# Optimization experiments

Measured on AMD Instinct MI355X. Metric: run time of the kernel, lower is better.

Reference implementation:

```python
import jax, jax.numpy as jnp
import numpy as np

ALPHA = 0.2            # LeakyReLU negative slope
NEG_BIG = -9e15        # mask fill value from the original code


def setup_inputs() -> dict:
    key = jax.random.key(0)
    k1, k2, k3, k4 = jax.random.split(key, 4)
    N, F_in, F_out = 8192, 512, 256
    x = jax.random.normal(k1, (N, F_in), dtype=jnp.float32)
    support = jax.random.randint(k2, (N, N), 0, 2, dtype=jnp.int32)  # dense 0/1 adjacency
    W = jax.random.normal(k3, (F_in, F_out), dtype=jnp.float32) * (1.0 / np.sqrt(F_in))
    a = jax.random.normal(k4, (2 * F_out, 1), dtype=jnp.float32) * 0.05
    return {"x": x, "support": support, "W": W, "a": a}


def _attention_logits(h, a):
    # Faithful reproduction of the ORIGINAL (buggy) torch layout:
    #   a_input = cat([h.repeat(1,N).view(N*N,-1), h.repeat(N,1)], dim=0).view(N, N, 2F)
    # Working out the flat-index arithmetic (N even):
    #   for i <  N/2: a_input[i,j] = concat(h[q], h[q]),  q = 2*i + (j >= N/2)
    #   for i >= N/2: a_input[i,j] = concat(h[(2j) % N], h[(2j+1) % N])   (independent of i)
    # so e_raw[i,j] = a_input[i,j] @ a decomposes via s = h@a1, t = h@a2.
    N, F = h.shape
    a1 = a[:F, 0]
    a2 = a[F:, 0]
    s = h @ a1                     # (N,)
    t = h @ a2                     # (N,)
    u = s + t
    half = N // 2
    j = jnp.arange(N)
    i_top = jnp.arange(half)
    q = 2 * i_top[:, None] + (j[None, :] >= half).astype(jnp.int32)  # (half, N)
    top = u[q]                                                       # rows i < N/2
    bot = s[(2 * j) % N] + t[(2 * j + 1) % N]                        # (N,) same for all i >= N/2
    e_raw = jnp.concatenate([top, jnp.broadcast_to(bot, (N - half, N))], axis=0)
    return jnp.where(e_raw > 0, e_raw, ALPHA * e_raw)  # LeakyReLU


def reference(x, support, W, a):
    h = x @ W                                  # (N, F_out)
    e = _attention_logits(h, a)                # (N, N)
    scores = jnp.where(support > 0, e, jnp.float32(NEG_BIG))
    attn = jax.nn.softmax(scores, axis=1)      # dropout p=0.0 -> identity
    h_out = attn @ h                           # (N, F_out)
    return jax.nn.elu(h_out)                   # concat=True
```

## Files before the change

kernel.cpp:

```cpp
#include <hip/hip_runtime.h>


typedef short bf16x8 __attribute__((ext_vector_type(8)));
typedef float f32x4 __attribute__((ext_vector_type(4)));

static __device__ __forceinline__ unsigned short f2bf(float f) {
    unsigned int u = __builtin_bit_cast(unsigned int, f);
    unsigned int r = (u + 0x7FFFu + ((u >> 16) & 1u)) >> 16;
    return (unsigned short)r;
}
static __device__ __forceinline__ float bf2f(unsigned short s) {
    unsigned int u = ((unsigned int)s) << 16;
    return __builtin_bit_cast(float, u);
}

__global__ __launch_bounds__(256) void k_cvt_x(const float* __restrict__ x,
                                               unsigned short* __restrict__ xb) {
    int i = (blockIdx.x * 256 + threadIdx.x) * 4;
    float4 v = *(const float4*)(x + i);
    ushort4 o = make_ushort4(f2bf(v.x), f2bf(v.y), f2bf(v.z), f2bf(v.w));
    *(ushort4*)(xb + i) = o;
}

__global__ __launch_bounds__(256) void k_cvt_w(const float* __restrict__ W,
                                               unsigned short* __restrict__ Wbt) {
    int idx = blockIdx.x * 256 + threadIdx.x;
    int n = idx >> 9, k = idx & 511;
    Wbt[idx] = f2bf(W[k * 256 + n]);
}

__global__ __launch_bounds__(256) void k_gemm_h(const unsigned short* __restrict__ xb,
                                                const unsigned short* __restrict__ Wbt,
                                                unsigned short* __restrict__ h,
                                                unsigned short* __restrict__ B1t) {
    __shared__ unsigned short Asm[128][72];
    __shared__ unsigned short Bsm[64][72];
    int tid = threadIdx.x;
    int wv = tid >> 6, ln = tid & 63;
    int m0 = blockIdx.x * 128, n0 = blockIdx.y * 64;

    f32x4 acc[2][4];
#pragma unroll
    for (int i = 0; i < 2; i++)
#pragma unroll
        for (int j = 0; j < 4; j++) acc[i][j] = (f32x4)0.0f;

    for (int k0 = 0; k0 < 512; k0 += 64) {
        {
            int r = tid >> 1, c = (tid & 1) * 32;
            const unsigned short* src = xb + (m0 + r) * 512 + k0 + c;
            *(bf16x8*)&Asm[r][c]      = *(const bf16x8*)(src);
            *(bf16x8*)&Asm[r][c + 8]  = *(const bf16x8*)(src + 8);
            *(bf16x8*)&Asm[r][c + 16] = *(const bf16x8*)(src + 16);
            *(bf16x8*)&Asm[r][c + 24] = *(const bf16x8*)(src + 24);
        }
        {
            int r = tid >> 2, c = (tid & 3) * 16;
            const unsigned short* src = Wbt + (n0 + r) * 512 + k0 + c;
            *(bf16x8*)&Bsm[r][c]     = *(const bf16x8*)(src);
            *(bf16x8*)&Bsm[r][c + 8] = *(const bf16x8*)(src + 8);
        }
        __syncthreads();
        int lr = ln & 15, lk = (ln >> 4) * 8;
#pragma unroll
        for (int ks = 0; ks < 2; ks++) {
            int kk = ks * 32 + lk;
            bf16x8 a0 = *(const bf16x8*)&Asm[wv * 32 + lr][kk];
            bf16x8 a1 = *(const bf16x8*)&Asm[wv * 32 + 16 + lr][kk];
#pragma unroll
            for (int nt = 0; nt < 4; nt++) {
                bf16x8 b = *(const bf16x8*)&Bsm[nt * 16 + lr][kk];
                acc[0][nt] = __builtin_amdgcn_mfma_f32_16x16x32_bf16(a0, b, acc[0][nt], 0, 0, 0);
                acc[1][nt] = __builtin_amdgcn_mfma_f32_16x16x32_bf16(a1, b, acc[1][nt], 0, 0, 0);
            }
        }
        __syncthreads();
    }
    int lr = ln & 15, lrow = (ln >> 4) * 4;
#pragma unroll
    for (int mt = 0; mt < 2; mt++) {
#pragma unroll
        for (int nt = 0; nt < 4; nt++) {
            int mg = m0 + wv * 32 + mt * 16 + lrow;
            int ng = n0 + nt * 16 + lr;
            ushort4 tb = make_ushort4(f2bf(acc[mt][nt][0]), f2bf(acc[mt][nt][1]),
                                      f2bf(acc[mt][nt][2]), f2bf(acc[mt][nt][3]));
            h[(mg + 0) * 256 + ng] = tb.x;
            h[(mg + 1) * 256 + ng] = tb.y;
            h[(mg + 2) * 256 + ng] = tb.z;
            h[(mg + 3) * 256 + ng] = tb.w;
            *(ushort4*)&B1t[ng * 8192 + mg] = tb;
        }
    }
}

__global__ __launch_bounds__(256) void k_st(const unsigned short* __restrict__ h,
                                            const float* __restrict__ a,
                                            float* __restrict__ s, float* __restrict__ t) {
    int wv = threadIdx.x >> 6, ln = threadIdx.x & 63;
    int j = blockIdx.x * 4 + wv;
    ushort4 hv = *(const ushort4*)(h + j * 256 + ln * 4);
    float4 a1 = *(const float4*)(a + ln * 4);
    float4 a2 = *(const float4*)(a + 256 + ln * 4);
    float s_ = bf2f(hv.x) * a1.x + bf2f(hv.y) * a1.y + bf2f(hv.z) * a1.z + bf2f(hv.w) * a1.w;
    float t_ = bf2f(hv.x) * a2.x + bf2f(hv.y) * a2.y + bf2f(hv.z) * a2.z + bf2f(hv.w) * a2.w;
#pragma unroll
    for (int off = 32; off; off >>= 1) {
        s_ += __shfl_down(s_, off);
        t_ += __shfl_down(t_, off);
    }
    if (ln == 0) { s[j] = s_; t[j] = t_; }
}

__global__ __launch_bounds__(256) void k_weights(const float* __restrict__ s,
                                                 const float* __restrict__ t,
                                                 float* __restrict__ wb,
                                                 float* __restrict__ eL,
                                                 float* __restrict__ eR,
                                                 unsigned short* __restrict__ B1t) {
    int j = blockIdx.x * 256 + threadIdx.x;
    float eb = s[(2 * j) & 8191] + t[(2 * j + 1) & 8191];
    eb = eb > 0.0f ? eb : 0.2f * eb;
    wb[j] = expf(eb);
    if (j < 4096) {
        float cL = s[2 * j] + t[2 * j];
        cL = cL > 0.0f ? cL : 0.2f * cL;
        float cR = s[2 * j + 1] + t[2 * j + 1];
        cR = cR > 0.0f ? cR : 0.2f * cR;
        eL[j] = expf(cL);
        eR[j] = expf(cR);
    }
    B1t[256 * 8192 + j] = 0x3F80;
#pragma unroll
    for (int f = 257; f < 272; f++) B1t[f * 8192 + j] = 0;
}

__global__ __launch_bounds__(256) void k_b2(const unsigned short* __restrict__ B1t,
                                            const float* __restrict__ wb,
                                            unsigned short* __restrict__ B2t) {
    int j = blockIdx.x * 256 + threadIdx.x;
    int f = blockIdx.y;
    B2t[f * 8192 + j] = f2bf(wb[j] * bf2f(B1t[f * 8192 + j]));
}

static __device__ __forceinline__ bf16x8 cvt01(int4 a, int4 b) {
    bf16x8 r;
    r[0] = a.x ? (short)0x3F80 : (short)0; r[1] = a.y ? (short)0x3F80 : (short)0;
    r[2] = a.z ? (short)0x3F80 : (short)0; r[3] = a.w ? (short)0x3F80 : (short)0;
    r[4] = b.x ? (short)0x3F80 : (short)0; r[5] = b.y ? (short)0x3F80 : (short)0;
    r[6] = b.z ? (short)0x3F80 : (short)0; r[7] = b.w ? (short)0x3F80 : (short)0;
    return r;
}

template <int NF>
static __device__ __forceinline__ void mg_body(unsigned short* __restrict__ As,
                                               const int* __restrict__ asrc,
                                               int arow, int acx,
                                               const unsigned short* __restrict__ bp,
                                               float* __restrict__ op, int ln) {
    f32x4 acc[2][NF];
#pragma unroll
    for (int i = 0; i < 2; i++)
#pragma unroll
        for (int j = 0; j < NF; j++) acc[i][j] = (f32x4)0.0f;

    {
        int4 a0 = *(const int4*)(asrc);
        int4 a1 = *(const int4*)(asrc + 4);
        *(bf16x8*)&As[arow * 72 + acx] = cvt01(a0, a1);
    }
    int r0 = (ln & 15), r1 = 16 + (ln & 15), lk = (ln >> 4) * 8;

#pragma unroll 1
    for (int it = 0; it < 32; ++it) {
        __syncthreads();
        int4 na0, na1;
        if (it < 31) {
            const int* a2 = asrc + (it + 1) * 64;
            na0 = *(const int4*)(a2);
            na1 = *(const int4*)(a2 + 4);
        }
        int base = (it & 1) * 32 * 72;
#pragma unroll
        for (int kh = 0; kh < 2; kh++) {
            bf16x8 af0 = *(const bf16x8*)&As[base + r0 * 72 + kh * 32 + lk];
            bf16x8 af1 = *(const bf16x8*)&As[base + r1 * 72 + kh * 32 + lk];
#pragma unroll
            for (int f = 0; f < NF; f++) {
                bf16x8 bv = *(const bf16x8*)(bp + (long)f * 131072 + it * 64 + kh * 32);
                acc[0][f] = __builtin_amdgcn_mfma_f32_16x16x32_bf16(af0, bv, acc[0][f], 0, 0, 0);
                acc[1][f] = __builtin_amdgcn_mfma_f32_16x16x32_bf16(af1, bv, acc[1][f], 0, 0, 0);
            }
        }
        if (it < 31) {
            int nb = ((it & 1) ^ 1) * 32 * 72;
            *(bf16x8*)&As[nb + arow * 72 + acx] = cvt01(na0, na1);
        }
    }
    int lr = ln & 15, lrow = (ln >> 4) * 4;
#pragma unroll
    for (int mf = 0; mf < 2; mf++)
#pragma unroll
        for (int f = 0; f < NF; f++)
#pragma unroll
            for (int r = 0; r < 4; r++)
                unsafeAtomicAdd(&op[(long)(mf * 16 + lrow + r) * 272 + f * 16 + lr],
                                acc[mf][f][r]);
}

__global__ __launch_bounds__(256, 4) void k_mgemm(const int* __restrict__ sup,
                                                  const unsigned short* __restrict__ B1t,
                                                  const unsigned short* __restrict__ B2t,
                                                  float* __restrict__ TL, float* __restrict__ TR,
                                                  float* __restrict__ TB0, float* __restrict__ TB1) {
    __shared__ unsigned short Asm[2 * 32 * 72];
    int tid = threadIdx.x;
    int wv = tid >> 6, ln = tid & 63;

    int bid = blockIdx.x + (blockIdx.y << 8);
    int xcd = bid & 7;
    int idx = bid >> 3;
    int q = xcd >> 1;
    int strip = (idx << 1) | (xcd & 1);

    bool topv = strip < 128;
    long m0 = (long)strip * 32;
    const unsigned short* Bt = topv ? B1t : B2t;
    float* out = topv ? ((q < 2) ? TL : TR) : ((q < 2) ? TB0 : TB1);
    long outr0 = topv ? m0 : m0 - 4096;
    long K0 = (long)q * 2048;
    int n0 = wv ? (4 * wv + 1) * 16 : 0;

    int arow = tid >> 3, acx = (tid & 7) * 8;
    const int* asrc = sup + (m0 + arow) * 8192 + K0 + acx;
    const unsigned short* bp = Bt + (long)(n0 + (ln & 15)) * 8192 + K0 + (ln >> 4) * 8;
    float* op = out + outr0 * 272 + n0;

    if (wv == 0) mg_body<5>(Asm, asrc, arow, acx, bp, op, ln);
    else         mg_body<4>(Asm, asrc, arow, acx, bp, op, ln);
}

__global__ __launch_bounds__(256) void k_out(const float* __restrict__ TL,
                                             const float* __restrict__ TR,
                                             const float* __restrict__ TB0,
                                             const float* __restrict__ TB1,
                                             const float* __restrict__ eL,
                                             const float* __restrict__ eR,
                                             float* __restrict__ outp) {
    int i = blockIdx.x, f = threadIdx.x;
    float num, den;
    if (i < 4096) {
        float el = eL[i], er = eR[i];
        den = el * TL[i * 272 + 256] + er * TR[i * 272 + 256];
        num = el * TL[i * 272 + f] + er * TR[i * 272 + f];
    } else {
        int ii = i - 4096;
        den = TB0[ii * 272 + 256] + TB1[ii * 272 + 256];
        num = TB0[ii * 272 + f] + TB1[ii * 272 + f];
    }
    float r = num / den;
    outp[i * 256 + f] = r > 0.0f ? r : expm1f(r);
}

extern "C" void kernel_launch(void* const* d_in, const int* in_sizes, int n_in,
                              void* d_out, int out_size, void* d_ws, size_t ws_size,
                              hipStream_t stream) {
    (void)in_sizes; (void)n_in; (void)out_size; (void)ws_size;
    const float* x = (const float*)d_in[0];
    const int* sup = (const int*)d_in[1];
    const float* W = (const float*)d_in[2];
    const float* a = (const float*)d_in[3];
    float* outp = (float*)d_out;

    char* ws = (char*)d_ws;
    size_t off = 0;
    auto alloc = [&](size_t bytes) -> void* {
        void* p = ws + off;
        off += (bytes + 255) & ~(size_t)255;
        return p;
    };
    unsigned short* xb  = (unsigned short*)alloc(8192 * 512 * 2);
    unsigned short* Wbt = (unsigned short*)alloc(256 * 512 * 2);
    unsigned short* h   = (unsigned short*)alloc(8192 * 256 * 2);
    unsigned short* B1t = (unsigned short*)alloc(272 * 8192 * 2);
    unsigned short* B2t = (unsigned short*)alloc(272 * 8192 * 2);
    float* s   = (float*)alloc(8192 * 4);
    float* t   = (float*)alloc(8192 * 4);
    float* wb  = (float*)alloc(8192 * 4);
    float* eL  = (float*)alloc(4096 * 4);
    float* eR  = (float*)alloc(4096 * 4);
    float* TL  = (float*)alloc(4096 * 272 * 4);
    float* TR  = (float*)alloc(4096 * 272 * 4);
    float* TB0 = (float*)alloc(4096 * 272 * 4);
    float* TB1 = (float*)alloc(4096 * 272 * 4);

    hipMemsetAsync(TL, 0, (size_t)4 * 4096 * 272 * 4, stream);

    k_cvt_x<<<4096, 256, 0, stream>>>(x, xb);
    k_cvt_w<<<512, 256, 0, stream>>>(W, Wbt);
    k_gemm_h<<<dim3(64, 4), 256, 0, stream>>>(xb, Wbt, h, B1t);
    k_st<<<2048, 256, 0, stream>>>(h, a, s, t);
    k_weights<<<32, 256, 0, stream>>>(s, t, wb, eL, eR, B1t);
    k_b2<<<dim3(32, 272), 256, 0, stream>>>(B1t, wb, B2t);
    k_mgemm<<<dim3(256, 4), 256, 0, stream>>>(sup, B1t, B2t, TL, TR, TB0, TB1);
    k_out<<<8192, 256, 0, stream>>>(TL, TR, TB0, TB1, eL, eR, outp);
}
```

Baseline: 212.0 us.

## Restructure mask GEMM: stage B via direct-to-LDS loads, split-K partials without atomics

The masked GEMM is restructured so each block handles a 64-row strip over a 1024-wide K slice. The B operand (272 columns) is staged in swizzled, double-buffered LDS using global_load_lds, and each wave converts its own adjacency fragment straight from registers. Atomic accumulation into four zero-initialized buffers is replaced by plain stores into 8 split-K partial buffers, which k_out then sums, so the memset goes away. The cost is a larger workspace and more reads in k_out, plus higher register pressure from 17 accumulators per wave.

```diff
diff --git a/kernel.cpp b/kernel.cpp
--- a/kernel.cpp
+++ b/kernel.cpp
@@ -12,6 +12,11 @@
 static __device__ __forceinline__ float bf2f(unsigned short s) {
     unsigned int u = ((unsigned int)s) << 16;
     return __builtin_bit_cast(float, u);
+}
+static __device__ __forceinline__ void glds16(const unsigned short* g, unsigned short* l) {
+    __builtin_amdgcn_global_load_lds(
+        (const __attribute__((address_space(1))) unsigned int*)(g),
+        (__attribute__((address_space(3))) unsigned int*)(l), 16, 0, 0);
 }
 
 __global__ __launch_bounds__(256) void k_cvt_x(const float* __restrict__ x,
@@ -152,114 +157,129 @@
     return r;
 }
 
-template <int NF>
-static __device__ __forceinline__ void mg_body(unsigned short* __restrict__ As,
-                                               const int* __restrict__ asrc,
-                                               int arow, int acx,
-                                               const unsigned short* __restrict__ bp,
-                                               float* __restrict__ op, int ln) {
-    f32x4 acc[2][NF];
-#pragma unroll
-    for (int i = 0; i < 2; i++)
-#pragma unroll
-        for (int j = 0; j < NF; j++) acc[i][j] = (f32x4)0.0f;
-
-    {
-        int4 a0 = *(const int4*)(asrc);
-        int4 a1 = *(const int4*)(asrc + 4);
-        *(bf16x8*)&As[arow * 72 + acx] = cvt01(a0, a1);
-    }
-    int r0 = (ln & 15), r1 = 16 + (ln & 15), lk = (ln >> 4) * 8;
-
-#pragma unroll 1
-    for (int it = 0; it < 32; ++it) {
-        __syncthreads();
-        int4 na0, na1;
-        if (it < 31) {
-            const int* a2 = asrc + (it + 1) * 64;
-            na0 = *(const int4*)(a2);
-            na1 = *(const int4*)(a2 + 4);
-        }
-        int base = (it & 1) * 32 * 72;
-#pragma unroll
-        for (int kh = 0; kh < 2; kh++) {
-            bf16x8 af0 = *(const bf16x8*)&As[base + r0 * 72 + kh * 32 + lk];
-            bf16x8 af1 = *(const bf16x8*)&As[base + r1 * 72 + kh * 32 + lk];
-#pragma unroll
-            for (int f = 0; f < NF; f++) {
-                bf16x8 bv = *(const bf16x8*)(bp + (long)f * 131072 + it * 64 + kh * 32);
-                acc[0][f] = __builtin_amdgcn_mfma_f32_16x16x32_bf16(af0, bv, acc[0][f], 0, 0, 0);
-                acc[1][f] = __builtin_amdgcn_mfma_f32_16x16x32_bf16(af1, bv, acc[1][f], 0, 0, 0);
-            }
-        }
-        if (it < 31) {
-            int nb = ((it & 1) ^ 1) * 32 * 72;
-            *(bf16x8*)&As[nb + arow * 72 + acx] = cvt01(na0, na1);
-        }
-    }
-    int lr = ln & 15, lrow = (ln >> 4) * 4;
-#pragma unroll
-    for (int mf = 0; mf < 2; mf++)
-#pragma unroll
-        for (int f = 0; f < NF; f++)
-#pragma unroll
-            for (int r = 0; r < 4; r++)
-                unsafeAtomicAdd(&op[(long)(mf * 16 + lrow + r) * 272 + f * 16 + lr],
-                                acc[mf][f][r]);
-}
-
 __global__ __launch_bounds__(256, 4) void k_mgemm(const int* __restrict__ sup,
                                                   const unsigned short* __restrict__ B1t,
                                                   const unsigned short* __restrict__ B2t,
-                                                  float* __restrict__ TL, float* __restrict__ TR,
-                                                  float* __restrict__ TB0, float* __restrict__ TB1) {
-    __shared__ unsigned short Asm[2 * 32 * 72];
-    int tid = threadIdx.x;
-    int wv = tid >> 6, ln = tid & 63;
-
-    int bid = blockIdx.x + (blockIdx.y << 8);
-    int xcd = bid & 7;
-    int idx = bid >> 3;
-    int q = xcd >> 1;
-    int strip = (idx << 1) | (xcd & 1);
-
-    bool topv = strip < 128;
-    long m0 = (long)strip * 32;
-    const unsigned short* Bt = topv ? B1t : B2t;
-    float* out = topv ? ((q < 2) ? TL : TR) : ((q < 2) ? TB0 : TB1);
-    long outr0 = topv ? m0 : m0 - 4096;
-    long K0 = (long)q * 2048;
-    int n0 = wv ? (4 * wv + 1) * 16 : 0;
-
-    int arow = tid >> 3, acx = (tid & 7) * 8;
-    const int* asrc = sup + (m0 + arow) * 8192 + K0 + acx;
-    const unsigned short* bp = Bt + (long)(n0 + (ln & 15)) * 8192 + K0 + (ln >> 4) * 8;
-    float* op = out + outr0 * 272 + n0;
-
-    if (wv == 0) mg_body<5>(Asm, asrc, arow, acx, bp, op, ln);
-    else         mg_body<4>(Asm, asrc, arow, acx, bp, op, ln);
-}
-
-__global__ __launch_bounds__(256) void k_out(const float* __restrict__ TL,
-                                             const float* __restrict__ TR,
-                                             const float* __restrict__ TB0,
-                                             const float* __restrict__ TB1,
+                                                  float* __restrict__ P) {
+    __shared__ unsigned short Bsm[2 * 8704];
+    int tid = threadIdx.x, wv = tid >> 6, ln = tid & 63;
+    int bid = blockIdx.x;
+    int q = bid & 7;
+    int strip = bid >> 3;
+    long K0 = (long)q * 1024;
+    long m0 = (long)strip * 64;
+    const unsigned short* Bt = (strip < 64) ? B1t : B2t;
+
+    const unsigned short* sp0; const unsigned short* sp1;
+    const unsigned short* sp2; const unsigned short* sp3;
+    const unsigned short* sp4;
+    int cb0, cb1, cb2, cb3, cb4;
+    {
+        int ch;
+#define SETUP_SP(I, SP, CB) \
+        ch = (I)*256 + wv*64 + ln; \
+        { int row = ch >> 2, c = ch & 3; \
+          CB = ((I)*256 + wv*64) * 8; \
+          SP = Bt + (long)row * 8192 + K0 + ((c ^ (row & 3)) << 3); }
+        SETUP_SP(0, sp0, cb0)
+        SETUP_SP(1, sp1, cb1)
+        SETUP_SP(2, sp2, cb2)
+        SETUP_SP(3, sp3, cb3)
+        ch = 1024 + ln;
+        { int row = ch >> 2, c = ch & 3;
+          cb4 = 1024 * 8;
+          sp4 = Bt + (long)row * 8192 + K0 + ((c ^ (row & 3)) << 3); }
+#undef SETUP_SP
+    }
+
+    const int* ap = sup + (m0 + wv * 16 + (ln & 15)) * 8192 + K0 + (ln >> 4) * 8;
+
+    f32x4 acc[17];
+#pragma unroll
+    for (int i = 0; i < 17; i++) acc[i] = (f32x4)0.0f;
+
+    {
+        unsigned short* dst = Bsm;
+        glds16(sp0, dst + cb0);
+        glds16(sp1, dst + cb1);
+        glds16(sp2, dst + cb2);
+        glds16(sp3, dst + cb3);
+        if (wv == 0) glds16(sp4, dst + cb4);
+    }
+    int4 c0 = *(const int4*)(ap);
+    int4 c1 = *(const int4*)(ap + 4);
+    int4 n0 = *(const int4*)(ap + 32);
+    int4 n1 = *(const int4*)(ap + 36);
+    int4 f0 = c0, f1 = c1;
+    asm volatile("s_waitcnt vmcnt(4)" ::: "memory");
+    __builtin_amdgcn_s_barrier();
+
+    int lr = ln & 15;
+    int swz16 = 16 * ((ln >> 4) ^ (ln & 3));
+
+#pragma unroll 1
+    for (int it = 0; it < 32; ++it) {
+        int buf = it & 1;
+        if (it < 31) {
+            unsigned short* dst = Bsm + (buf ^ 1) * 8704;
+            glds16(sp0 + (it + 1) * 32, dst + cb0);
+            glds16(sp1 + (it + 1) * 32, dst + cb1);
+            glds16(sp2 + (it + 1) * 32, dst + cb2);
+            glds16(sp3 + (it + 1) * 32, dst + cb3);
+            if (wv == 0) glds16(sp4 + (it + 1) * 32, dst + cb4);
+        }
+        if (it < 30) {
+            f0 = *(const int4*)(ap + (it + 2) * 32);
+            f1 = *(const int4*)(ap + (it + 2) * 32 + 4);
+        }
+        bf16x8 av = cvt01(c0, c1);
+        const char* base = (const char*)Bsm + buf * 17408 + 64 * lr + swz16;
+#pragma unroll
+        for (int f = 0; f < 17; f++) {
+            bf16x8 bv = *(const bf16x8*)(base + f * 1024);
+            acc[f] = __builtin_amdgcn_mfma_f32_16x16x32_bf16(av, bv, acc[f], 0, 0, 0);
+        }
+        c0 = n0; c1 = n1; n0 = f0; n1 = f1;
+        if (it < 31) {
+            if (it < 30) asm volatile("s_waitcnt vmcnt(2)" ::: "memory");
+            else         asm volatile("s_waitcnt vmcnt(0)" ::: "memory");
+            __builtin_amdgcn_s_barrier();
+        }
+    }
+
+    long grow = m0 + wv * 16 + (ln >> 4) * 4;
+    float* op = P + ((long)q * 8192 + grow) * 272 + lr;
+#pragma unroll
+    for (int f = 0; f < 17; f++)
+#pragma unroll
+        for (int r = 0; r < 4; r++)
+            op[(long)r * 272 + f * 16] = acc[f][r];
+}
+
+__global__ __launch_bounds__(256) void k_out(const float* __restrict__ P,
                                              const float* __restrict__ eL,
                                              const float* __restrict__ eR,
                                              float* __restrict__ outp) {
     int i = blockIdx.x, f = threadIdx.x;
+    const float* p = P + (long)i * 272;
+    const long QS = 8192l * 272;
     float num, den;
     if (i < 4096) {
+        float tln = 0, trn = 0, tld = 0, trd = 0;
+#pragma unroll
+        for (int q = 0; q < 4; q++) { tln += p[q * QS + f]; tld += p[q * QS + 256]; }
+#pragma unroll
+        for (int q = 4; q < 8; q++) { trn += p[q * QS + f]; trd += p[q * QS + 256]; }
         float el = eL[i], er = eR[i];
-        den = el * TL[i * 272 + 256] + er * TR[i * 272 + 256];
-        num = el * TL[i * 272 + f] + er * TR[i * 272 + f];
+        num = el * tln + er * trn;
+        den = el * tld + er * trd;
     } else {
-        int ii = i - 4096;
-        den = TB0[ii * 272 + 256] + TB1[ii * 272 + 256];
-        num = TB0[ii * 272 + f] + TB1[ii * 272 + f];
+        num = 0; den = 0;
+#pragma unroll
+        for (int q = 0; q < 8; q++) { num += p[q * QS + f]; den += p[q * QS + 256]; }
     }
     float r = num / den;
-    outp[i * 256 + f] = r > 0.0f ? r : expm1f(r);
+    outp[(long)i * 256 + f] = r > 0.0f ? r : expm1f(r);
 }
 
 extern "C" void kernel_launch(void* const* d_in, const int* in_sizes, int n_in,
@@ -289,12 +309,7 @@
     float* wb  = (float*)alloc(8192 * 4);
     float* eL  = (float*)alloc(4096 * 4);
     float* eR  = (float*)alloc(4096 * 4);
-    float* TL  = (float*)alloc(4096 * 272 * 4);
-    float* TR  = (float*)alloc(4096 * 272 * 4);
-    float* TB0 = (float*)alloc(4096 * 272 * 4);
-    float* TB1 = (float*)alloc(4096 * 272 * 4);
-
-    hipMemsetAsync(TL, 0, (size_t)4 * 4096 * 272 * 4, stream);
+    float* P   = (float*)alloc((size_t)8 * 8192 * 272 * 4);
 
     k_cvt_x<<<4096, 256, 0, stream>>>(x, xb);
     k_cvt_w<<<512, 256, 0, stream>>>(W, Wbt);
@@ -302,6 +317,6 @@
     k_st<<<2048, 256, 0, stream>>>(h, a, s, t);
     k_weights<<<32, 256, 0, stream>>>(s, t, wb, eL, eR, B1t);
     k_b2<<<dim3(32, 272), 256, 0, stream>>>(B1t, wb, B2t);
-    k_mgemm<<<dim3(256, 4), 256, 0, stream>>>(sup, B1t, B2t, TL, TR, TB0, TB1);
-    k_out<<<8192, 256, 0, stream>>>(TL, TR, TB0, TB1, eL, eR, outp);
-}
+    k_mgemm<<<1024, 256, 0, stream>>>(sup, B1t, B2t, P);
+    k_out<<<8192, 256, 0, stream>>>(P, eL, eR, outp);
+}
```

Result: faster. 186.5 us (-12.0%).
